# Kernel tuning notes

Measured on AMD Instinct MI355X. Metric: run time of the kernel, lower is better.

## Reference

```python
import jax, jax.numpy as jnp
import numpy as np

DIM_H = 128
HEADS = 8
HEAD_DIM = DIM_H // HEADS
N_NODES = 40000
N_EDGES = 640000
BN_EPS = 1e-5


def setup_inputs() -> dict:
    key = jax.random.key(0)
    ks = jax.random.split(key, 16)
    s = 0.05
    x = jax.random.normal(ks[0], (N_NODES, DIM_H), dtype=jnp.float32)
    edge_index = jax.random.randint(ks[1], (2, N_EDGES), 0, N_NODES, dtype=jnp.int64)
    p = lambda k, shp: jax.random.normal(k, shp, dtype=jnp.float32) * s
    return {
        "x": x,
        "edge_index": edge_index,
        "Wk": p(ks[2], (DIM_H, DIM_H)), "bk": p(ks[3], (DIM_H,)),
        "Wv": p(ks[4], (DIM_H, DIM_H)), "bv": p(ks[5], (DIM_H,)),
        "Wo": p(ks[6], (DIM_H, DIM_H)), "bo": p(ks[7], (DIM_H,)),
        "bn1_g": jnp.ones((DIM_H,), jnp.float32), "bn1_b": jnp.zeros((DIM_H,), jnp.float32),
        "W1": p(ks[8], (2 * DIM_H, DIM_H)), "b1": p(ks[9], (2 * DIM_H,)),
        "W2": p(ks[10], (DIM_H, 2 * DIM_H)), "b2": p(ks[11], (DIM_H,)),
        "bn2_g": jnp.ones((DIM_H,), jnp.float32), "bn2_b": jnp.zeros((DIM_H,), jnp.float32),
    }


def _batchnorm(h, gamma, beta):
    # BatchNorm1d in training mode: per-feature batch mean / biased var over nodes
    mu = jnp.mean(h, axis=0)
    var = jnp.mean((h - mu) ** 2, axis=0)
    return (h - mu) * jax.lax.rsqrt(var + BN_EPS) * gamma + beta


def _sparse_attn(x, edge_index, Wk, bk, Wv, bv, Wo, bo):
    N = x.shape[0]
    src, dst = edge_index[0], edge_index[1]
    K = (x @ Wk.T + bk).reshape(N, HEADS, HEAD_DIM)
    V = (x @ Wv.T + bv).reshape(N, HEADS, HEAD_DIM)
    Q = x.reshape(N, HEADS, HEAD_DIM)  # query is raw h (no projection)
    # per-edge scores [E, H]
    scores = jnp.sum(K[src] * Q[dst], axis=-1) / np.sqrt(HEAD_DIM).astype(np.float32)
    # segment softmax over destination nodes (pyg_softmax)
    m = jax.ops.segment_max(scores, dst, num_segments=N)
    e = jnp.exp(scores - m[dst])
    denom = jax.ops.segment_sum(e, dst, num_segments=N)
    attn = e / (denom[dst] + 1e-16)  # [E, H]
    messages = V[src] * attn[:, :, None]  # [E, H, D]
    out = jax.ops.segment_sum(messages, dst, num_segments=N)  # [N, H, D]
    return out.reshape(N, DIM_H) @ Wo.T + bo


def reference(x, edge_index, Wk, bk, Wv, bv, Wo, bo, bn1_g, bn1_b,
              W1, b1, W2, b2, bn2_g, bn2_b):
    h_attn = _sparse_attn(x, edge_index, Wk, bk, Wv, bv, Wo, bo)
    h = _batchnorm(x + h_attn, bn1_g, bn1_b)
    ff = jax.nn.relu(h @ W1.T + b1) @ W2.T + b2
    h = _batchnorm(h + ff, bn2_g, bn2_b)
    return h
```

## Files before the change

### kernel.cpp

```cpp
#include <hip/hip_runtime.h>

#define DIM 128
#define NSHARD 8

typedef __attribute__((ext_vector_type(2))) float f32x2;
typedef __attribute__((ext_vector_type(4))) _Float16 half4;
typedef __attribute__((ext_vector_type(8))) _Float16 half8;
typedef __attribute__((ext_vector_type(4))) float f32x4;

#define HP 136
#define UP 264

__device__ __forceinline__ unsigned char to_fp8(float v) {
  return (unsigned char)(__builtin_amdgcn_cvt_pk_fp8_f32(v, v, 0, false) & 0xff);
}

__global__ __launch_bounds__(256) void conv_wall(const float* __restrict__ Wk,
    const float* __restrict__ Wv, const float* __restrict__ Wo,
    const float* __restrict__ W1, const float* __restrict__ W2,
    _Float16* __restrict__ Wkh, _Float16* __restrict__ Wvh,
    _Float16* __restrict__ Woh, _Float16* __restrict__ W1h,
    _Float16* __restrict__ W2h, int* __restrict__ cnt, float* __restrict__ stats,
    int N) {
  int i = blockIdx.x * 256 + threadIdx.x;
  int nth = gridDim.x * 256;
  if (i < 16384) Wkh[i] = (_Float16)Wk[i];
  else if (i < 32768) Wvh[i - 16384] = (_Float16)Wv[i - 16384];
  else if (i < 49152) Woh[i - 32768] = (_Float16)Wo[i - 32768];
  else if (i < 81920) W1h[i - 49152] = (_Float16)W1[i - 49152];
  else if (i < 114688) W2h[i - 81920] = (_Float16)W2[i - 81920];
  for (int j = i; j < N * NSHARD; j += nth) cnt[j] = 0;
  if (i < 512) stats[i] = 0.f;
}

__global__ __launch_bounds__(256) void kv_mfma(const float* __restrict__ x,
    const _Float16* __restrict__ Wkh, const float* __restrict__ bk,
    const _Float16* __restrict__ Wvh, const float* __restrict__ bv,
    unsigned char* __restrict__ KV8, int N) {
  __shared__ _Float16 xs[64 * HP];
  int tid = threadIdx.x;
  int base = blockIdx.x * 64;
  int lane = tid & 63, w = tid >> 6;
  int l15 = lane & 15, quad = lane >> 4;

  for (int i = tid; i < 64 * 32; i += 256) {
    int m = i >> 5, c4 = i & 31;
    float4 tv = ((const float4*)x)[(size_t)(base + m) * 32 + c4];
    half4 hv;
    hv.x = (_Float16)tv.x; hv.y = (_Float16)tv.y;
    hv.z = (_Float16)tv.z; hv.w = (_Float16)tv.w;
    *(half4*)&xs[m * HP + c4 * 4] = hv;
  }
  __syncthreads();

  half8 afr[4][4];
#pragma unroll
  for (int mt = 0; mt < 4; mt++)
#pragma unroll
    for (int ks = 0; ks < 4; ks++)
      afr[mt][ks] = *(const half8*)&xs[(mt * 16 + l15) * HP + ks * 32 + quad * 8];

  const _Float16* W = (w < 2) ? Wkh : Wvh;
  const float* bias = (w < 2) ? bk : bv;
  int voff = (w < 2) ? 0 : 4;
  int c0 = (w & 1) * 64;

#pragma unroll
  for (int nt = 0; nt < 4; nt++) {
    int f = c0 + nt * 16 + l15;
    half8 bfr[4];
#pragma unroll
    for (int ks = 0; ks < 4; ks++)
      bfr[ks] = *(const half8*)&W[(size_t)f * 128 + ks * 32 + quad * 8];
    f32x4 acc[4];
#pragma unroll
    for (int mt = 0; mt < 4; mt++) acc[mt] = (f32x4){0.f, 0.f, 0.f, 0.f};
#pragma unroll
    for (int ks = 0; ks < 4; ks++)
#pragma unroll
      for (int mt = 0; mt < 4; mt++)
        acc[mt] = __builtin_amdgcn_mfma_f32_16x16x32_f16(afr[mt][ks], bfr[ks],
                                                          acc[mt], 0, 0, 0);
    float bb = bias[f];
    int fo = (f >> 2) * 8 + (f & 3) + voff;
#pragma unroll
    for (int mt = 0; mt < 4; mt++)
#pragma unroll
      for (int r = 0; r < 4; r++)
        KV8[(size_t)(base + mt * 16 + quad * 4 + r) * 256 + fo] =
            to_fp8(acc[mt][r] + bb);
  }
}

__global__ __launch_bounds__(256) void hist_rank(const int* __restrict__ ei,
    int* __restrict__ cnt, int* __restrict__ rank, int N, int E) {
  int e = blockIdx.x * 256 + threadIdx.x;
  if (e < E) rank[e] = atomicAdd(&cnt[(e & (NSHARD - 1)) * N + ei[E + e]], 1);
}

__global__ __launch_bounds__(256) void scanA(const int* __restrict__ cnt,
    int* __restrict__ rs, int* __restrict__ bsum, int N) {
  __shared__ int s[256];
  int t = threadIdx.x;
  int i = blockIdx.x * 256 + t;
  int v = 0;
  if (i < N)
#pragma unroll
    for (int sh = 0; sh < NSHARD; sh++) v += cnt[sh * N + i];
  s[t] = v;
  __syncthreads();
  for (int off = 1; off < 256; off <<= 1) {
    int add = (t >= off) ? s[t - off] : 0;
    __syncthreads();
    s[t] += add;
    __syncthreads();
  }
  if (i < N) rs[i] = s[t] - v;
  if (t == 255) bsum[blockIdx.x] = s[t];
}

__global__ __launch_bounds__(256) void scanB(int* __restrict__ bsum, int nb) {
  __shared__ int s[256];
  int t = threadIdx.x;
  int v = (t < nb) ? bsum[t] : 0;
  s[t] = v;
  __syncthreads();
  for (int off = 1; off < 256; off <<= 1) {
    int add = (t >= off) ? s[t - off] : 0;
    __syncthreads();
    s[t] += add;
    __syncthreads();
  }
  if (t < nb) bsum[t] = s[t] - v;
}

__global__ __launch_bounds__(256) void scanC(int* __restrict__ rs,
    const int* __restrict__ bsum, const int* __restrict__ cnt,
    int* __restrict__ rs_shard, int N, int E) {
  int i = blockIdx.x * 256 + threadIdx.x;
  if (i < N) {
    int b = rs[i] + bsum[blockIdx.x];
    rs[i] = b;
#pragma unroll
    for (int sh = 0; sh < NSHARD; sh++) {
      rs_shard[sh * N + i] = b;
      b += cnt[sh * N + i];
    }
  }
  if (i == 0) rs[N] = E;
}

__global__ __launch_bounds__(256) void scatter2(const int* __restrict__ ei,
    const int* __restrict__ rs_shard, const int* __restrict__ rank,
    int* __restrict__ esrc, int N, int E) {
  int e = blockIdx.x * 256 + threadIdx.x;
  if (e < E)
    esrc[rs_shard[(e & (NSHARD - 1)) * N + ei[E + e]] + rank[e]] = ei[e];
}

__global__ __launch_bounds__(256) void attn_agg(const unsigned char* __restrict__ KV8,
    const float* __restrict__ x, const int* __restrict__ rs,
    const int* __restrict__ esrc, _Float16* __restrict__ attn16, int N) {
  int wave = threadIdx.x >> 6, lane = threadIdx.x & 63;
  int n = blockIdx.x * 4 + wave;
  if (n >= N) return;
  int l = lane & 31, s = lane >> 5;
  float4 q = *(const float4*)&x[(size_t)n * DIM + 4 * l];
  int beg = rs[n], end = rs[n + 1];
  float a0 = 0.f, a1 = 0.f, a2 = 0.f, a3 = 0.f, dloc = 0.f;
  for (int e = beg + s; e < end; e += 8) {
    bool hh[4];
    int ss[4];
#pragma unroll
    for (int u = 0; u < 4; u++) hh[u] = (e + 2 * u) < end;
    ss[0] = esrc[e];
#pragma unroll
    for (int u = 1; u < 4; u++) ss[u] = hh[u] ? esrc[e + 2 * u] : ss[0];
    uint2 kv[4];
#pragma unroll
    for (int u = 0; u < 4; u++)
      kv[u] = *(const uint2*)&KV8[(size_t)ss[u] * 256 + 8 * l];
    float p[4];
#pragma unroll
    for (int u = 0; u < 4; u++) {
      f32x2 k01 = __builtin_amdgcn_cvt_pk_f32_fp8(kv[u].x, false);
      f32x2 k23 = __builtin_amdgcn_cvt_pk_f32_fp8(kv[u].x, true);
      p[u] = k01[0] * q.x + k01[1] * q.y + k23[0] * q.z + k23[1] * q.w;
    }
#pragma unroll
    for (int u = 0; u < 4; u++) p[u] += __shfl_xor(p[u], 1);
#pragma unroll
    for (int u = 0; u < 4; u++) p[u] += __shfl_xor(p[u], 2);
#pragma unroll
    for (int u = 0; u < 4; u++) {
      float ev = hh[u] ? __expf(p[u] * 0.25f) : 0.f;
      dloc += ev;
      f32x2 v01 = __builtin_amdgcn_cvt_pk_f32_fp8(kv[u].y, false);
      f32x2 v23 = __builtin_amdgcn_cvt_pk_f32_fp8(kv[u].y, true);
      a0 += ev * v01[0];
      a1 += ev * v01[1];
      a2 += ev * v23[0];
      a3 += ev * v23[1];
    }
  }
  dloc += __shfl_xor(dloc, 32);
  a0 += __shfl_xor(a0, 32);
  a1 += __shfl_xor(a1, 32);
  a2 += __shfl_xor(a2, 32);
  a3 += __shfl_xor(a3, 32);
  if (s == 0) {
    float inv = 1.0f / (dloc + 1e-16f);
    half4 o;
    o.x = (_Float16)(a0 * inv);
    o.y = (_Float16)(a1 * inv);
    o.z = (_Float16)(a2 * inv);
    o.w = (_Float16)(a3 * inv);
    *(half4*)&attn16[(size_t)n * DIM + 4 * l] = o;
  }
}

__global__ __launch_bounds__(256) void o_proj_mfma(const _Float16* __restrict__ attn16,
    const float* __restrict__ x, const _Float16* __restrict__ Woh,
    const float* __restrict__ bo, float* __restrict__ t,
    float* __restrict__ stats, int N) {
  __shared__ _Float16 as16[64 * HP];
  int tid = threadIdx.x;
  int base = blockIdx.x * 64;
  int lane = tid & 63, w = tid >> 6;
  int l15 = lane & 15, quad = lane >> 4;

  for (int i = tid; i < 64 * 16; i += 256) {
    int m = i >> 4, c8 = i & 15;
    *(half8*)&as16[m * HP + c8 * 8] =
        ((const half8*)attn16)[(size_t)(base + m) * 16 + c8];
  }
  __syncthreads();

  half8 afr[4][4];
#pragma unroll
  for (int mt = 0; mt < 4; mt++)
#pragma unroll
    for (int ks = 0; ks < 4; ks++)
      afr[mt][ks] = *(const half8*)&as16[(mt * 16 + l15) * HP + ks * 32 + quad * 8];

  int c0 = w * 32;
  f32x4 acc[4][2];
#pragma unroll
  for (int mt = 0; mt < 4; mt++)
#pragma unroll
    for (int nt = 0; nt < 2; nt++) acc[mt][nt] = (f32x4){0.f, 0.f, 0.f, 0.f};
#pragma unroll
  for (int ks = 0; ks < 4; ks++) {
    half8 b[2];
#pragma unroll
    for (int nt = 0; nt < 2; nt++)
      b[nt] = *(const half8*)&Woh[(size_t)(c0 + nt * 16 + l15) * 128 + ks * 32 +
                                  quad * 8];
#pragma unroll
    for (int mt = 0; mt < 4; mt++)
#pragma unroll
      for (int nt = 0; nt < 2; nt++)
        acc[mt][nt] =
            __builtin_amdgcn_mfma_f32_16x16x32_f16(afr[mt][ks], b[nt], acc[mt][nt], 0, 0, 0);
  }

#pragma unroll
  for (int nt = 0; nt < 2; nt++) {
    int f = c0 + nt * 16 + l15;
    float bb = bo[f];
    float s = 0.f, q = 0.f;
#pragma unroll
    for (int mt = 0; mt < 4; mt++) {
#pragma unroll
      for (int r = 0; r < 4; r++) {
        int row = mt * 16 + quad * 4 + r;
        float tv = acc[mt][nt][r] + bb + x[(size_t)(base + row) * DIM + f];
        t[(size_t)(base + row) * DIM + f] = tv;
        s += tv;
        q += tv * tv;
      }
    }
    s += __shfl_xor(s, 16);
    s += __shfl_xor(s, 32);
    q += __shfl_xor(q, 16);
    q += __shfl_xor(q, 32);
    if (quad == 0) {
      atomicAdd(&stats[f], s);
      atomicAdd(&stats[128 + f], q);
    }
  }
}

__global__ __launch_bounds__(256) void ffn_mfma(const float* __restrict__ t,
    const float* __restrict__ stats1, const float* __restrict__ g1,
    const float* __restrict__ bb1, const _Float16* __restrict__ W1h,
    const float* __restrict__ b1, const _Float16* __restrict__ W2h,
    const float* __restrict__ b2, float* __restrict__ z,
    float* __restrict__ stats2, float invN, int N) {
  __shared__ _Float16 hs[64 * HP];
  __shared__ _Float16 us[64 * UP];
  __shared__ float cf[256];
  int tid = threadIdx.x;
  int base = blockIdx.x * 64;
  int lane = tid & 63, w = tid >> 6;
  int l15 = lane & 15, quad = lane >> 4;

  if (tid < 128) {
    float mu = stats1[tid] * invN;
    float var = stats1[128 + tid] * invN - mu * mu;
    float a = rsqrtf(var + 1e-5f) * g1[tid];
    cf[tid] = a;
    cf[128 + tid] = bb1[tid] - mu * a;
  }
  __syncthreads();

  for (int i = tid; i < 64 * 32; i += 256) {
    int m = i >> 5, c4 = i & 31;
    float4 tv = ((const float4*)t)[(size_t)(base + m) * 32 + c4];
    float4 ca = ((const float4*)cf)[c4];
    float4 cc = ((const float4*)cf)[32 + c4];
    half4 hv;
    hv.x = (_Float16)(tv.x * ca.x + cc.x);
    hv.y = (_Float16)(tv.y * ca.y + cc.y);
    hv.z = (_Float16)(tv.z * ca.z + cc.z);
    hv.w = (_Float16)(tv.w * ca.w + cc.w);
    *(half4*)&hs[m * HP + c4 * 4] = hv;
  }
  __syncthreads();

  int n0 = w * 64;
  half8 afr[4][4];
#pragma unroll
  for (int mt = 0; mt < 4; mt++)
#pragma unroll
    for (int ks = 0; ks < 4; ks++)
      afr[mt][ks] = *(const half8*)&hs[(mt * 16 + l15) * HP + ks * 32 + quad * 8];

#pragma unroll
  for (int nt = 0; nt < 4; nt++) {
    int n = n0 + nt * 16 + l15;
    half8 bfr[4];
#pragma unroll
    for (int ks = 0; ks < 4; ks++)
      bfr[ks] = *(const half8*)&W1h[(size_t)n * 128 + ks * 32 + quad * 8];
    f32x4 acc[4];
#pragma unroll
    for (int mt = 0; mt < 4; mt++) acc[mt] = (f32x4){0.f, 0.f, 0.f, 0.f};
#pragma unroll
    for (int ks = 0; ks < 4; ks++)
#pragma unroll
      for (int mt = 0; mt < 4; mt++)
        acc[mt] = __builtin_amdgcn_mfma_f32_16x16x32_f16(afr[mt][ks], bfr[ks],
                                                          acc[mt], 0, 0, 0);
    float bias = b1[n];
#pragma unroll
    for (int mt = 0; mt < 4; mt++)
#pragma unroll
      for (int r = 0; r < 4; r++)
        us[(mt * 16 + quad * 4 + r) * UP + n] =
            (_Float16)fmaxf(acc[mt][r] + bias, 0.f);
  }
  __syncthreads();

  int n2 = w * 32;
  f32x4 acc2[4][2];
#pragma unroll
  for (int mt = 0; mt < 4; mt++)
#pragma unroll
    for (int nt = 0; nt < 2; nt++) acc2[mt][nt] = (f32x4){0.f, 0.f, 0.f, 0.f};
  for (int ks = 0; ks < 8; ks++) {
    half8 a[4], b[2];
#pragma unroll
    for (int mt = 0; mt < 4; mt++)
      a[mt] = *(const half8*)&us[(mt * 16 + l15) * UP + ks * 32 + quad * 8];
#pragma unroll
    for (int nt = 0; nt < 2; nt++)
      b[nt] = *(const half8*)&W2h[(size_t)(n2 + nt * 16 + l15) * 256 + ks * 32 +
                                  quad * 8];
#pragma unroll
    for (int mt = 0; mt < 4; mt++)
#pragma unroll
      for (int nt = 0; nt < 2; nt++)
        acc2[mt][nt] =
            __builtin_amdgcn_mfma_f32_16x16x32_f16(a[mt], b[nt], acc2[mt][nt], 0, 0, 0);
  }

#pragma unroll
  for (int nt = 0; nt < 2; nt++) {
    int f = n2 + nt * 16 + l15;
    float bz = b2[f];
    float s = 0.f, q = 0.f;
#pragma unroll
    for (int mt = 0; mt < 4; mt++) {
#pragma unroll
      for (int r = 0; r < 4; r++) {
        int row = mt * 16 + quad * 4 + r;
        float hv = (float)hs[row * HP + f];
        float zv = hv + acc2[mt][nt][r] + bz;
        z[(size_t)(base + row) * DIM + f] = zv;
        s += zv;
        q += zv * zv;
      }
    }
    s += __shfl_xor(s, 16);
    s += __shfl_xor(s, 32);
    q += __shfl_xor(q, 16);
    q += __shfl_xor(q, 32);
    if (quad == 0) {
      atomicAdd(&stats2[f], s);
      atomicAdd(&stats2[128 + f], q);
    }
  }
}

__global__ __launch_bounds__(256) void final_apply(const float* __restrict__ z,
    const float* __restrict__ stats2, const float* __restrict__ g2,
    const float* __restrict__ bb2, float* __restrict__ out, float invN,
    int total4) {
  __shared__ float cf[256];
  int tid = threadIdx.x;
  if (tid < 128) {
    float mu = stats2[tid] * invN;
    float var = stats2[128 + tid] * invN - mu * mu;
    float a = rsqrtf(var + 1e-5f) * g2[tid];
    cf[tid] = a;
    cf[128 + tid] = bb2[tid] - mu * a;
  }
  __syncthreads();
  int i = blockIdx.x * 256 + tid;
  if (i >= total4) return;
  int f = (i * 4) & 127;
  float4 zv = ((const float4*)z)[i];
  float4 o;
  o.x = zv.x * cf[f] + cf[128 + f];
  o.y = zv.y * cf[f + 1] + cf[128 + f + 1];
  o.z = zv.z * cf[f + 2] + cf[128 + f + 2];
  o.w = zv.w * cf[f + 3] + cf[128 + f + 3];
  ((float4*)out)[i] = o;
}

extern "C" void kernel_launch(void* const* d_in, const int* in_sizes, int n_in,
                              void* d_out, int out_size, void* d_ws, size_t ws_size,
                              hipStream_t stream) {
  const float* x = (const float*)d_in[0];
  const int* ei = (const int*)d_in[1];
  const float* Wk = (const float*)d_in[2];
  const float* bk = (const float*)d_in[3];
  const float* Wv = (const float*)d_in[4];
  const float* bv = (const float*)d_in[5];
  const float* Wo = (const float*)d_in[6];
  const float* bo = (const float*)d_in[7];
  const float* bn1_g = (const float*)d_in[8];
  const float* bn1_b = (const float*)d_in[9];
  const float* W1 = (const float*)d_in[10];
  const float* b1 = (const float*)d_in[11];
  const float* W2 = (const float*)d_in[12];
  const float* b2 = (const float*)d_in[13];
  const float* bn2_g = (const float*)d_in[14];
  const float* bn2_b = (const float*)d_in[15];
  float* out = (float*)d_out;

  int N = in_sizes[0] / DIM;
  int E = in_sizes[1] / 2;

  unsigned char* KV8 = (unsigned char*)d_ws;
  _Float16* attn16 = (_Float16*)(KV8 + (size_t)N * 256);
  float* zbuf = (float*)(attn16 + (size_t)N * DIM);
  float* tbuf = zbuf + (size_t)N * DIM;
  _Float16* W1h = (_Float16*)(tbuf + (size_t)N * DIM);
  _Float16* W2h = W1h + 32768;
  _Float16* Wkh = W2h + 32768;
  _Float16* Wvh = Wkh + 16384;
  _Float16* Woh = Wvh + 16384;
  float* stats = (float*)(Woh + 16384);
  int* cnt = (int*)(stats + 512);
  int* rs = cnt + (size_t)N * NSHARD;
  int* rs_shard = rs + N + 1;
  int* rank = rs_shard + (size_t)N * NSHARD;
  int* esrc = rank + E;
  int* bsum = esrc + E;

  int nblk = (N + 255) / 256;
  float invN = 1.0f / N;

  conv_wall<<<512, 256, 0, stream>>>(Wk, Wv, Wo, W1, W2, Wkh, Wvh, Woh, W1h, W2h,
                                     cnt, stats, N);
  kv_mfma<<<N / 64, 256, 0, stream>>>(x, Wkh, bk, Wvh, bv, KV8, N);
  hist_rank<<<(E + 255) / 256, 256, 0, stream>>>(ei, cnt, rank, N, E);
  scanA<<<nblk, 256, 0, stream>>>(cnt, rs, bsum, N);
  scanB<<<1, 256, 0, stream>>>(bsum, nblk);
  scanC<<<nblk, 256, 0, stream>>>(rs, bsum, cnt, rs_shard, N, E);
  scatter2<<<(E + 255) / 256, 256, 0, stream>>>(ei, rs_shard, rank, esrc, N, E);
  attn_agg<<<(N + 3) / 4, 256, 0, stream>>>(KV8, x, rs, esrc, attn16, N);
  o_proj_mfma<<<N / 64, 256, 0, stream>>>(attn16, x, Woh, bo, tbuf, stats, N);
  ffn_mfma<<<N / 64, 256, 0, stream>>>(tbuf, stats, bn1_g, bn1_b, W1h, b1, W2h, b2,
                                       zbuf, stats + 256, invN, N);
  final_apply<<<((N * DIM / 4) + 255) / 256, 256, 0, stream>>>(
      zbuf, stats + 256, bn2_g, bn2_b, out, invN, N * DIM / 4);
}
```

Baseline: 249.4 us.

## Fuse CSR build and BatchNorm passes into persistent kernels with grid barriers

Merges the weight conversion, histogram, three scan stages and scatter into one kernel that uses software grid barriers instead of separate launches. It also folds each BatchNorm apply into the preceding GEMM kernel: tiles stay in shared memory (as fp16) across a grid-wide barrier once the global statistics are ready. This removes several launches and the fp32 t/z round trips through global memory. The barriers assume all 625 (or 640) blocks are co-resident, which risks deadlock or a timeout break if occupancy is too low, and the kept tiles now carry fp16 rounding.

```diff
diff --git a/kernel.cpp b/kernel.cpp
--- a/kernel.cpp
+++ b/kernel.cpp
@@ -15,22 +15,102 @@
   return (unsigned char)(__builtin_amdgcn_cvt_pk_fp8_f32(v, v, 0, false) & 0xff);
 }
 
-__global__ __launch_bounds__(256) void conv_wall(const float* __restrict__ Wk,
-    const float* __restrict__ Wv, const float* __restrict__ Wo,
-    const float* __restrict__ W1, const float* __restrict__ W2,
-    _Float16* __restrict__ Wkh, _Float16* __restrict__ Wvh,
-    _Float16* __restrict__ Woh, _Float16* __restrict__ W1h,
-    _Float16* __restrict__ W2h, int* __restrict__ cnt, float* __restrict__ stats,
-    int N) {
-  int i = blockIdx.x * 256 + threadIdx.x;
+__device__ __forceinline__ void grid_bar(unsigned* ctr, unsigned target) {
+  __syncthreads();
+  if (threadIdx.x == 0) {
+    __threadfence();
+    __hip_atomic_fetch_add(ctr, 1u, __ATOMIC_RELEASE, __HIP_MEMORY_SCOPE_AGENT);
+    unsigned spin = 0;
+    while (__hip_atomic_load(ctr, __ATOMIC_ACQUIRE, __HIP_MEMORY_SCOPE_AGENT) <
+           target) {
+      if (++spin > 20000000u) break;
+      __builtin_amdgcn_s_sleep(1);
+    }
+    __threadfence();
+  }
+  __syncthreads();
+}
+
+__global__ __launch_bounds__(256, 4) void csr_coop(
+    const float* __restrict__ Wk, const float* __restrict__ Wv,
+    const float* __restrict__ Wo, const float* __restrict__ W1,
+    const float* __restrict__ W2, _Float16* __restrict__ Wkh,
+    _Float16* __restrict__ Wvh, _Float16* __restrict__ Woh,
+    _Float16* __restrict__ W1h, _Float16* __restrict__ W2h,
+    float* __restrict__ stats, const int* __restrict__ ei,
+    int* __restrict__ cnt, int* __restrict__ rank, int* __restrict__ rs,
+    int* __restrict__ rs_shard, int* __restrict__ esrc, int* __restrict__ bsum,
+    unsigned* __restrict__ gb, int N, int E) {
+  __shared__ int s[256];
+  int t = threadIdx.x;
+  int gtid = blockIdx.x * 256 + t;
   int nth = gridDim.x * 256;
-  if (i < 16384) Wkh[i] = (_Float16)Wk[i];
-  else if (i < 32768) Wvh[i - 16384] = (_Float16)Wv[i - 16384];
-  else if (i < 49152) Woh[i - 32768] = (_Float16)Wo[i - 32768];
-  else if (i < 81920) W1h[i - 49152] = (_Float16)W1[i - 49152];
-  else if (i < 114688) W2h[i - 81920] = (_Float16)W2[i - 81920];
-  for (int j = i; j < N * NSHARD; j += nth) cnt[j] = 0;
-  if (i < 512) stats[i] = 0.f;
+  unsigned nblk = gridDim.x;
+
+  if (gtid < 16384) Wkh[gtid] = (_Float16)Wk[gtid];
+  else if (gtid < 32768) Wvh[gtid - 16384] = (_Float16)Wv[gtid - 16384];
+  else if (gtid < 49152) Woh[gtid - 32768] = (_Float16)Wo[gtid - 32768];
+  else if (gtid < 81920) W1h[gtid - 49152] = (_Float16)W1[gtid - 49152];
+  else if (gtid < 114688) W2h[gtid - 81920] = (_Float16)W2[gtid - 81920];
+  for (int j = gtid; j < N * NSHARD; j += nth) cnt[j] = 0;
+  if (gtid < 512) stats[gtid] = 0.f;
+  grid_bar(&gb[0], nblk);
+
+  for (int e = gtid; e < E; e += nth)
+    rank[e] = atomicAdd(&cnt[(e & (NSHARD - 1)) * N + ei[E + e]], 1);
+  grid_bar(&gb[1], nblk);
+
+  int nblk2 = (N + 255) >> 8;
+  if ((int)blockIdx.x < nblk2) {
+    int i = blockIdx.x * 256 + t;
+    int v = 0;
+    if (i < N)
+#pragma unroll
+      for (int sh = 0; sh < NSHARD; sh++) v += cnt[sh * N + i];
+    s[t] = v;
+    __syncthreads();
+    for (int off = 1; off < 256; off <<= 1) {
+      int add = (t >= off) ? s[t - off] : 0;
+      __syncthreads();
+      s[t] += add;
+      __syncthreads();
+    }
+    if (i < N) rs[i] = s[t] - v;
+    if (t == 255) bsum[blockIdx.x] = s[t];
+  }
+  grid_bar(&gb[2], nblk);
+
+  if (blockIdx.x == 0) {
+    int v = (t < nblk2) ? bsum[t] : 0;
+    s[t] = v;
+    __syncthreads();
+    for (int off = 1; off < 256; off <<= 1) {
+      int add = (t >= off) ? s[t - off] : 0;
+      __syncthreads();
+      s[t] += add;
+      __syncthreads();
+    }
+    if (t < nblk2) bsum[t] = s[t] - v;
+  }
+  grid_bar(&gb[3], nblk);
+
+  if ((int)blockIdx.x < nblk2) {
+    int i = blockIdx.x * 256 + t;
+    if (i < N) {
+      int b = rs[i] + bsum[blockIdx.x];
+      rs[i] = b;
+#pragma unroll
+      for (int sh = 0; sh < NSHARD; sh++) {
+        rs_shard[sh * N + i] = b;
+        b += cnt[sh * N + i];
+      }
+    }
+    if (i == 0) rs[N] = E;
+  }
+  grid_bar(&gb[4], nblk);
+
+  for (int e = gtid; e < E; e += nth)
+    esrc[rs_shard[(e & (NSHARD - 1)) * N + ei[E + e]] + rank[e]] = ei[e];
 }
 
 __global__ __launch_bounds__(256) void kv_mfma(const float* __restrict__ x,
@@ -90,72 +170,6 @@
         KV8[(size_t)(base + mt * 16 + quad * 4 + r) * 256 + fo] =
             to_fp8(acc[mt][r] + bb);
   }
-}
-
-__global__ __launch_bounds__(256) void hist_rank(const int* __restrict__ ei,
-    int* __restrict__ cnt, int* __restrict__ rank, int N, int E) {
-  int e = blockIdx.x * 256 + threadIdx.x;
-  if (e < E) rank[e] = atomicAdd(&cnt[(e & (NSHARD - 1)) * N + ei[E + e]], 1);
-}
-
-__global__ __launch_bounds__(256) void scanA(const int* __restrict__ cnt,
-    int* __restrict__ rs, int* __restrict__ bsum, int N) {
-  __shared__ int s[256];
-  int t = threadIdx.x;
-  int i = blockIdx.x * 256 + t;
-  int v = 0;
-  if (i < N)
-#pragma unroll
-    for (int sh = 0; sh < NSHARD; sh++) v += cnt[sh * N + i];
-  s[t] = v;
-  __syncthreads();
-  for (int off = 1; off < 256; off <<= 1) {
-    int add = (t >= off) ? s[t - off] : 0;
-    __syncthreads();
-    s[t] += add;
-    __syncthreads();
-  }
-  if (i < N) rs[i] = s[t] - v;
-  if (t == 255) bsum[blockIdx.x] = s[t];
-}
-
-__global__ __launch_bounds__(256) void scanB(int* __restrict__ bsum, int nb) {
-  __shared__ int s[256];
-  int t = threadIdx.x;
-  int v = (t < nb) ? bsum[t] : 0;
-  s[t] = v;
-  __syncthreads();
-  for (int off = 1; off < 256; off <<= 1) {
-    int add = (t >= off) ? s[t - off] : 0;
-    __syncthreads();
-    s[t] += add;
-    __syncthreads();
-  }
-  if (t < nb) bsum[t] = s[t] - v;
-}
-
-__global__ __launch_bounds__(256) void scanC(int* __restrict__ rs,
-    const int* __restrict__ bsum, const int* __restrict__ cnt,
-    int* __restrict__ rs_shard, int N, int E) {
-  int i = blockIdx.x * 256 + threadIdx.x;
-  if (i < N) {
-    int b = rs[i] + bsum[blockIdx.x];
-    rs[i] = b;
-#pragma unroll
-    for (int sh = 0; sh < NSHARD; sh++) {
-      rs_shard[sh * N + i] = b;
-      b += cnt[sh * N + i];
-    }
-  }
-  if (i == 0) rs[N] = E;
-}
-
-__global__ __launch_bounds__(256) void scatter2(const int* __restrict__ ei,
-    const int* __restrict__ rs_shard, const int* __restrict__ rank,
-    int* __restrict__ esrc, int N, int E) {
-  int e = blockIdx.x * 256 + threadIdx.x;
-  if (e < E)
-    esrc[rs_shard[(e & (NSHARD - 1)) * N + ei[E + e]] + rank[e]] = ei[e];
 }
 
 __global__ __launch_bounds__(256) void attn_agg(const unsigned char* __restrict__ KV8,
@@ -219,11 +233,14 @@
   }
 }
 
-__global__ __launch_bounds__(256) void o_proj_mfma(const _Float16* __restrict__ attn16,
-    const float* __restrict__ x, const _Float16* __restrict__ Woh,
-    const float* __restrict__ bo, float* __restrict__ t,
-    float* __restrict__ stats, int N) {
+__global__ __launch_bounds__(256, 3) void o_proj_coop(
+    const _Float16* __restrict__ attn16, const float* __restrict__ x,
+    const _Float16* __restrict__ Woh, const float* __restrict__ bo,
+    const float* __restrict__ g1, const float* __restrict__ bb1,
+    _Float16* __restrict__ h16, float* __restrict__ stats,
+    unsigned* __restrict__ gb, float invN, int N) {
   __shared__ _Float16 as16[64 * HP];
+  __shared__ float cf[256];
   int tid = threadIdx.x;
   int base = blockIdx.x * 64;
   int lane = tid & 63, w = tid >> 6;
@@ -242,6 +259,7 @@
 #pragma unroll
     for (int ks = 0; ks < 4; ks++)
       afr[mt][ks] = *(const half8*)&as16[(mt * 16 + l15) * HP + ks * 32 + quad * 8];
+  __syncthreads();
 
   int c0 = w * 32;
   f32x4 acc[4][2];
@@ -275,7 +293,7 @@
       for (int r = 0; r < 4; r++) {
         int row = mt * 16 + quad * 4 + r;
         float tv = acc[mt][nt][r] + bb + x[(size_t)(base + row) * DIM + f];
-        t[(size_t)(base + row) * DIM + f] = tv;
+        as16[row * HP + f] = (_Float16)tv;
         s += tv;
         q += tv * tv;
       }
@@ -289,14 +307,37 @@
       atomicAdd(&stats[128 + f], q);
     }
   }
-}
-
-__global__ __launch_bounds__(256) void ffn_mfma(const float* __restrict__ t,
-    const float* __restrict__ stats1, const float* __restrict__ g1,
-    const float* __restrict__ bb1, const _Float16* __restrict__ W1h,
+
+  grid_bar(gb, 625);
+
+  if (tid < 128) {
+    float mu = stats[tid] * invN;
+    float var = stats[128 + tid] * invN - mu * mu;
+    float a = rsqrtf(var + 1e-5f) * g1[tid];
+    cf[tid] = a;
+    cf[128 + tid] = bb1[tid] - mu * a;
+  }
+  __syncthreads();
+
+  for (int i = tid; i < 64 * 16; i += 256) {
+    int m = i >> 4, c8 = i & 15;
+    half8 tv = *(const half8*)&as16[m * HP + c8 * 8];
+    half8 hv;
+#pragma unroll
+    for (int j = 0; j < 8; j++) {
+      int f = c8 * 8 + j;
+      hv[j] = (_Float16)((float)tv[j] * cf[f] + cf[128 + f]);
+    }
+    ((half8*)h16)[(size_t)(base + m) * 16 + c8] = hv;
+  }
+}
+
+__global__ __launch_bounds__(256, 3) void ffn_coop(
+    const _Float16* __restrict__ h16, const _Float16* __restrict__ W1h,
     const float* __restrict__ b1, const _Float16* __restrict__ W2h,
-    const float* __restrict__ b2, float* __restrict__ z,
-    float* __restrict__ stats2, float invN, int N) {
+    const float* __restrict__ b2, const float* __restrict__ g2,
+    const float* __restrict__ bb2, float* __restrict__ out,
+    float* __restrict__ stats2, unsigned* __restrict__ gb, float invN, int N) {
   __shared__ _Float16 hs[64 * HP];
   __shared__ _Float16 us[64 * UP];
   __shared__ float cf[256];
@@ -305,26 +346,10 @@
   int lane = tid & 63, w = tid >> 6;
   int l15 = lane & 15, quad = lane >> 4;
 
-  if (tid < 128) {
-    float mu = stats1[tid] * invN;
-    float var = stats1[128 + tid] * invN - mu * mu;
-    float a = rsqrtf(var + 1e-5f) * g1[tid];
-    cf[tid] = a;
-    cf[128 + tid] = bb1[tid] - mu * a;
-  }
-  __syncthreads();
-
-  for (int i = tid; i < 64 * 32; i += 256) {
-    int m = i >> 5, c4 = i & 31;
-    float4 tv = ((const float4*)t)[(size_t)(base + m) * 32 + c4];
-    float4 ca = ((const float4*)cf)[c4];
-    float4 cc = ((const float4*)cf)[32 + c4];
-    half4 hv;
-    hv.x = (_Float16)(tv.x * ca.x + cc.x);
-    hv.y = (_Float16)(tv.y * ca.y + cc.y);
-    hv.z = (_Float16)(tv.z * ca.z + cc.z);
-    hv.w = (_Float16)(tv.w * ca.w + cc.w);
-    *(half4*)&hs[m * HP + c4 * 4] = hv;
+  for (int i = tid; i < 64 * 16; i += 256) {
+    int m = i >> 4, c8 = i & 15;
+    *(half8*)&hs[m * HP + c8 * 8] =
+        ((const half8*)h16)[(size_t)(base + m) * 16 + c8];
   }
   __syncthreads();
 
@@ -397,7 +422,7 @@
         int row = mt * 16 + quad * 4 + r;
         float hv = (float)hs[row * HP + f];
         float zv = hv + acc2[mt][nt][r] + bz;
-        z[(size_t)(base + row) * DIM + f] = zv;
+        hs[row * HP + f] = (_Float16)zv;
         s += zv;
         q += zv * zv;
       }
@@ -411,14 +436,9 @@
       atomicAdd(&stats2[128 + f], q);
     }
   }
-}
-
-__global__ __launch_bounds__(256) void final_apply(const float* __restrict__ z,
-    const float* __restrict__ stats2, const float* __restrict__ g2,
-    const float* __restrict__ bb2, float* __restrict__ out, float invN,
-    int total4) {
-  __shared__ float cf[256];
-  int tid = threadIdx.x;
+
+  grid_bar(gb, 625);
+
   if (tid < 128) {
     float mu = stats2[tid] * invN;
     float var = stats2[128 + tid] * invN - mu * mu;
@@ -427,16 +447,24 @@
     cf[128 + tid] = bb2[tid] - mu * a;
   }
   __syncthreads();
-  int i = blockIdx.x * 256 + tid;
-  if (i >= total4) return;
-  int f = (i * 4) & 127;
-  float4 zv = ((const float4*)z)[i];
-  float4 o;
-  o.x = zv.x * cf[f] + cf[128 + f];
-  o.y = zv.y * cf[f + 1] + cf[128 + f + 1];
-  o.z = zv.z * cf[f + 2] + cf[128 + f + 2];
-  o.w = zv.w * cf[f + 3] + cf[128 + f + 3];
-  ((float4*)out)[i] = o;
+
+  for (int i = tid; i < 64 * 16; i += 256) {
+    int m = i >> 4, c8 = i & 15;
+    half8 zv = *(const half8*)&hs[m * HP + c8 * 8];
+    int f0 = c8 * 8;
+    float4 o1, o2;
+    o1.x = (float)zv[0] * cf[f0 + 0] + cf[128 + f0 + 0];
+    o1.y = (float)zv[1] * cf[f0 + 1] + cf[128 + f0 + 1];
+    o1.z = (float)zv[2] * cf[f0 + 2] + cf[128 + f0 + 2];
+    o1.w = (float)zv[3] * cf[f0 + 3] + cf[128 + f0 + 3];
+    o2.x = (float)zv[4] * cf[f0 + 4] + cf[128 + f0 + 4];
+    o2.y = (float)zv[5] * cf[f0 + 5] + cf[128 + f0 + 5];
+    o2.z = (float)zv[6] * cf[f0 + 6] + cf[128 + f0 + 6];
+    o2.w = (float)zv[7] * cf[f0 + 7] + cf[128 + f0 + 7];
+    size_t ob = (size_t)(base + m) * 32 + c8 * 2;
+    ((float4*)out)[ob] = o1;
+    ((float4*)out)[ob + 1] = o2;
+  }
 }
 
 extern "C" void kernel_launch(void* const* d_in, const int* in_sizes, int n_in,
@@ -465,9 +493,8 @@
 
   unsigned char* KV8 = (unsigned char*)d_ws;
   _Float16* attn16 = (_Float16*)(KV8 + (size_t)N * 256);
-  float* zbuf = (float*)(attn16 + (size_t)N * DIM);
-  float* tbuf = zbuf + (size_t)N * DIM;
-  _Float16* W1h = (_Float16*)(tbuf + (size_t)N * DIM);
+  _Float16* h16 = attn16 + (size_t)N * DIM;
+  _Float16* W1h = h16 + (size_t)N * DIM;
   _Float16* W2h = W1h + 32768;
   _Float16* Wkh = W2h + 32768;
   _Float16* Wvh = Wkh + 16384;
@@ -479,22 +506,20 @@
   int* rank = rs_shard + (size_t)N * NSHARD;
   int* esrc = rank + E;
   int* bsum = esrc + E;
-
-  int nblk = (N + 255) / 256;
+  unsigned* gb = (unsigned*)(bsum + 256);
+
   float invN = 1.0f / N;
-
-  conv_wall<<<512, 256, 0, stream>>>(Wk, Wv, Wo, W1, W2, Wkh, Wvh, Woh, W1h, W2h,
-                                     cnt, stats, N);
-  kv_mfma<<<N / 64, 256, 0, stream>>>(x, Wkh, bk, Wvh, bv, KV8, N);
-  hist_rank<<<(E + 255) / 256, 256, 0, stream>>>(ei, cnt, rank, N, E);
-  scanA<<<nblk, 256, 0, stream>>>(cnt, rs, bsum, N);
-  scanB<<<1, 256, 0, stream>>>(bsum, nblk);
-  scanC<<<nblk, 256, 0, stream>>>(rs, bsum, cnt, rs_shard, N, E);
-  scatter2<<<(E + 255) / 256, 256, 0, stream>>>(ei, rs_shard, rank, esrc, N, E);
+  float* stats2 = stats + 256;
+  int nwg = N / 64;
+
+  hipMemsetAsync(gb, 0, 8 * sizeof(unsigned), stream);
+  csr_coop<<<640, 256, 0, stream>>>(Wk, Wv, Wo, W1, W2, Wkh, Wvh, Woh, W1h,
+                                    W2h, stats, ei, cnt, rank, rs, rs_shard,
+                                    esrc, bsum, gb, N, E);
+  kv_mfma<<<nwg, 256, 0, stream>>>(x, Wkh, bk, Wvh, bv, KV8, N);
   attn_agg<<<(N + 3) / 4, 256, 0, stream>>>(KV8, x, rs, esrc, attn16, N);
-  o_proj_mfma<<<N / 64, 256, 0, stream>>>(attn16, x, Woh, bo, tbuf, stats, N);
-  ffn_mfma<<<N / 64, 256, 0, stream>>>(tbuf, stats, bn1_g, bn1_b, W1h, b1, W2h, b2,
-                                       zbuf, stats + 256, invN, N);
-  final_apply<<<((N * DIM / 4) + 255) / 256, 256, 0, stream>>>(
-      zbuf, stats + 256, bn2_g, bn2_b, out, invN, N * DIM / 4);
-}
+  o_proj_coop<<<nwg, 256, 0, stream>>>(attn16, x, Woh, bo, bn1_g, bn1_b, h16,
+                                       stats, &gb[5], invN, N);
+  ffn_coop<<<nwg, 256, 0, stream>>>(h16, W1h, b1, W2h, b2, bn2_g, bn2_b, out,
+                                    stats2, &gb[6], invN, N);
+}
```

New measurement: 823.5 us. +230.2%, slower.
